# Kernel optimization log

Hardware: AMD Instinct MI355X
Metric: run time of the kernel (lower is better)

The kernel has to match this reference:

```python
import jax, jax.numpy as jnp
import numpy as np

NUM_HEADS = 16
HEAD_SIZE = 64
N_EMBD = 1024


def setup_inputs() -> dict:
    key = jax.random.key(0)
    ks = jax.random.split(key, 6)
    B, T, C = 2, 2048, N_EMBD
    scale = 0.02
    return {
        "x": jax.random.normal(ks[0], (B, T, C), dtype=jnp.float32),
        "Wq": jax.random.normal(ks[1], (C, NUM_HEADS * HEAD_SIZE), dtype=jnp.float32) * scale,
        "Wk": jax.random.normal(ks[2], (C, NUM_HEADS * HEAD_SIZE), dtype=jnp.float32) * scale,
        "Wv": jax.random.normal(ks[3], (C, NUM_HEADS * HEAD_SIZE), dtype=jnp.float32) * scale,
        "Wo": jax.random.normal(ks[4], (NUM_HEADS * HEAD_SIZE, C), dtype=jnp.float32) * scale,
        "bo": jnp.zeros((C,), dtype=jnp.float32),
    }


def reference(x, Wq, Wk, Wv, Wo, bo):
    B, T, C = x.shape
    H, D = NUM_HEADS, HEAD_SIZE
    # QKV projections (no bias), reshape to [B, H, T, D]
    q = (x @ Wq).reshape(B, T, H, D).transpose(0, 2, 1, 3)
    k = (x @ Wk).reshape(B, T, H, D).transpose(0, 2, 1, 3)
    v = (x @ Wv).reshape(B, T, H, D).transpose(0, 2, 1, 3)
    # scaled dot-product scores [B, H, T, T]
    scores = jnp.einsum("bhqd,bhkd->bhqk", q, k) / jnp.sqrt(jnp.float32(D))
    causal = jnp.tril(jnp.ones((T, T), dtype=bool))
    scores = jnp.where(causal, scores, -jnp.inf)
    weights = jax.nn.softmax(scores, axis=-1)  # dropout = identity (eval)
    out = jnp.einsum("bhqk,bhkd->bhqd", weights, v)
    out = out.transpose(0, 2, 1, 3).reshape(B, T, H * D)
    return out @ Wo + bo
```

## Files before the change

kernel.cpp:

```cpp
#include <hip/hip_runtime.h>

typedef __attribute__((ext_vector_type(8))) _Float16 f16x8;
typedef __attribute__((ext_vector_type(4))) _Float16 f16x4;
typedef __attribute__((ext_vector_type(2))) _Float16 f16x2;
typedef __attribute__((ext_vector_type(2))) __fp16   fp16x2_raw;
typedef __attribute__((ext_vector_type(4))) float    f32x4;

#define NUM_HEADS 16
#define HEAD_D 64
#define EMB 1024
#define SEQ 2048
#define BATCH 2
#define MTOT (BATCH * SEQ)

#define QALPHA 0.18033688011112042f

__device__ __forceinline__ f16x2 cvt_pk_f16(float lo, float hi)
{
    fp16x2_raw r = __builtin_amdgcn_cvt_pkrtz(lo, hi);
    return __builtin_bit_cast(f16x2, r);
}

#if defined(__has_builtin)
#if __has_builtin(__builtin_amdgcn_exp2f)
#define HAVE_EXP2 1
#endif
#endif
__device__ __forceinline__ float fast_exp2(float x)
{
#ifdef HAVE_EXP2
    return __builtin_amdgcn_exp2f(x);
#else
    return __expf(x * 0.6931471805599453f);
#endif
}

#if defined(__has_builtin)
#if __has_builtin(__builtin_amdgcn_global_load_lds)
#define HAVE_GLOAD_LDS 1
#endif
#endif

__device__ __forceinline__ void stage16(const void* g, void* ldsWaveBase, int lane)
{
#ifdef HAVE_GLOAD_LDS
    __builtin_amdgcn_global_load_lds(
        (const __attribute__((address_space(1))) void*)g,
        (__attribute__((address_space(3))) void*)ldsWaveBase, 16, 0, 0);
    (void)lane;
#else
    *(f16x8*)((char*)ldsWaveBase + lane * 16) = *(const f16x8*)g;
#endif
}

__global__ __launch_bounds__(256) void prep_all(
    const float* __restrict__ x,
    const float* __restrict__ Wq, const float* __restrict__ Wk,
    const float* __restrict__ Wv, const float* __restrict__ Wo,
    _Float16* __restrict__ xh, _Float16* __restrict__ Wt,
    _Float16* __restrict__ Wto)
{
    const int z = blockIdx.z;
    if (z == 4) {
        int base = ((blockIdx.y * 32 + blockIdx.x) * 256 + threadIdx.x) * 2;
        #pragma unroll
        for (int t = 0; t < 2; ++t) {
            int i = base + t;
            float4 a = ((const float4*)x)[i * 2];
            float4 b = ((const float4*)x)[i * 2 + 1];
            f16x8 o;
            o[0] = (_Float16)a.x; o[1] = (_Float16)a.y;
            o[2] = (_Float16)a.z; o[3] = (_Float16)a.w;
            o[4] = (_Float16)b.x; o[5] = (_Float16)b.y;
            o[6] = (_Float16)b.z; o[7] = (_Float16)b.w;
            ((f16x8*)xh)[i] = o;
        }
        return;
    }
    const float* W = z == 0 ? Wq : (z == 1 ? Wk : (z == 2 ? Wv : Wo));
    _Float16* D = (z == 3) ? Wto : (Wt + (size_t)z * EMB * EMB);
    __shared__ float tile[32][33];
    const int tx = threadIdx.x & 31, ty = threadIdx.x >> 5;
    const int n0 = blockIdx.x * 32, k0 = blockIdx.y * 32;
    #pragma unroll
    for (int j = 0; j < 4; ++j)
        tile[ty + j * 8][tx] = W[(size_t)(k0 + ty + j * 8) * EMB + n0 + tx];
    __syncthreads();
    #pragma unroll
    for (int j = 0; j < 4; ++j)
        D[(size_t)(n0 + ty + j * 8) * EMB + k0 + tx] =
            (_Float16)tile[tx][ty + j * 8];
}

__global__ __launch_bounds__(256) void gemm_qkv(
    const _Float16* __restrict__ A, const _Float16* __restrict__ Bt,
    _Float16* __restrict__ Qh, _Float16* __restrict__ Kh,
    _Float16* __restrict__ VhT)
{
    __shared__ __align__(16) _Float16 As[128 * 32];
    __shared__ __align__(16) _Float16 Bs[128 * 32];

    const int tid = threadIdx.x;
    const int w = tid >> 6, lane = tid & 63;
    const int l15 = lane & 15, g4 = lane >> 4;
    const int wm = w >> 1, wn = w & 1;

    const int wg = blockIdx.y * gridDim.x + blockIdx.x;
    const int t  = (wg & 7) * 96 + (wg >> 3);
    const int bx = t >> 5, by = t & 31;
    const int row0 = by * 128, col0 = bx * 128;

    f32x4 acc[4][4];
    #pragma unroll
    for (int mt = 0; mt < 4; ++mt)
        #pragma unroll
        for (int nt = 0; nt < 4; ++nt)
            acc[mt][nt] = (f32x4){0.f, 0.f, 0.f, 0.f};

    for (int k0 = 0; k0 < EMB; k0 += 32) {
        __syncthreads();
        #pragma unroll
        for (int i = 0; i < 2; ++i) {
            int c = (i << 8) + tid;
            int row = c >> 2, u = c & 3;
            stage16(&A[(size_t)(row0 + row) * EMB + k0 + (u << 3)],
                    (char*)As + (i << 12) + (w << 10), lane);
            stage16(&Bt[(size_t)(col0 + row) * EMB + k0 + (u << 3)],
                    (char*)Bs + (i << 12) + (w << 10), lane);
        }
        __syncthreads();

        f16x8 af[4], bf[4];
        #pragma unroll
        for (int mt = 0; mt < 4; ++mt)
            af[mt] = *(const f16x8*)((const char*)As +
                     ((wm << 6) + (mt << 4) + l15) * 64 + (g4 << 4));
        #pragma unroll
        for (int nt = 0; nt < 4; ++nt)
            bf[nt] = *(const f16x8*)((const char*)Bs +
                     ((wn << 6) + (nt << 4) + l15) * 64 + (g4 << 4));
        #pragma unroll
        for (int mt = 0; mt < 4; ++mt)
            #pragma unroll
            for (int nt = 0; nt < 4; ++nt)
                acc[mt][nt] = __builtin_amdgcn_mfma_f32_16x16x32_f16(
                    af[mt], bf[nt], acc[mt][nt], 0, 0, 0);
    }

    #pragma unroll
    for (int mt = 0; mt < 4; ++mt) {
        int m = row0 + (wm << 6) + (mt << 4) + (g4 << 2);
        #pragma unroll
        for (int nt = 0; nt < 4; ++nt) {
            int gcol = col0 + (wn << 6) + (nt << 4) + l15;
            int proj = gcol >> 10, pc = gcol & 1023;
            int h = pc >> 6, d = pc & 63;
            int b = m >> 11, tt = m & 2047;
            int bh = b * NUM_HEADS + h;
            if (proj == 2) {
                f16x4 v4;
                v4[0] = (_Float16)acc[mt][nt][0];
                v4[1] = (_Float16)acc[mt][nt][1];
                v4[2] = (_Float16)acc[mt][nt][2];
                v4[3] = (_Float16)acc[mt][nt][3];
                *(f16x4*)&VhT[((size_t)bh * HEAD_D + d) * SEQ + tt] = v4;
            } else {
                _Float16* dst = proj == 0 ? Qh : Kh;
                float alpha = proj == 0 ? QALPHA : 1.0f;
                #pragma unroll
                for (int r = 0; r < 4; ++r)
                    dst[((size_t)bh * SEQ + tt + r) * HEAD_D + d] =
                        (_Float16)(acc[mt][nt][r] * alpha);
            }
        }
    }
}

__global__ __launch_bounds__(256) void gemm_out(
    const _Float16* __restrict__ A, const _Float16* __restrict__ Bt,
    float* __restrict__ outf, const float* __restrict__ bias)
{
    __shared__ __align__(16) _Float16 As[128 * 32];
    __shared__ __align__(16) _Float16 Bs[64 * 32];

    const int tid = threadIdx.x;
    const int w = tid >> 6, lane = tid & 63;
    const int l15 = lane & 15, g4 = lane >> 4;
    const int wm = w >> 1, wn = w & 1;

    const int wg = blockIdx.y * gridDim.x + blockIdx.x;
    const int t  = (wg & 7) * 64 + (wg >> 3);
    const int bx = t >> 5, by = t & 31;
    const int row0 = by * 128, col0 = bx * 64;

    f32x4 acc[4][2];
    #pragma unroll
    for (int mt = 0; mt < 4; ++mt)
        #pragma unroll
        for (int nt = 0; nt < 2; ++nt)
            acc[mt][nt] = (f32x4){0.f, 0.f, 0.f, 0.f};

    for (int k0 = 0; k0 < EMB; k0 += 32) {
        __syncthreads();
        #pragma unroll
        for (int i = 0; i < 2; ++i) {
            int c = (i << 8) + tid;
            int row = c >> 2, u = c & 3;
            stage16(&A[(size_t)(row0 + row) * EMB + k0 + (u << 3)],
                    (char*)As + (i << 12) + (w << 10), lane);
        }
        {
            int row = tid >> 2, u = tid & 3;
            stage16(&Bt[(size_t)(col0 + row) * EMB + k0 + (u << 3)],
                    (char*)Bs + (w << 10), lane);
        }
        __syncthreads();

        f16x8 af[4], bf[2];
        #pragma unroll
        for (int mt = 0; mt < 4; ++mt)
            af[mt] = *(const f16x8*)((const char*)As +
                     ((wm << 6) + (mt << 4) + l15) * 64 + (g4 << 4));
        #pragma unroll
        for (int nt = 0; nt < 2; ++nt)
            bf[nt] = *(const f16x8*)((const char*)Bs +
                     ((wn << 5) + (nt << 4) + l15) * 64 + (g4 << 4));
        #pragma unroll
        for (int mt = 0; mt < 4; ++mt)
            #pragma unroll
            for (int nt = 0; nt < 2; ++nt)
                acc[mt][nt] = __builtin_amdgcn_mfma_f32_16x16x32_f16(
                    af[mt], bf[nt], acc[mt][nt], 0, 0, 0);
    }

    #pragma unroll
    for (int mt = 0; mt < 4; ++mt) {
        int m = row0 + (wm << 6) + (mt << 4) + (g4 << 2);
        #pragma unroll
        for (int nt = 0; nt < 2; ++nt) {
            int gcol = col0 + (wn << 5) + (nt << 4) + l15;
            float bz = bias[gcol];
            #pragma unroll
            for (int r = 0; r < 4; ++r)
                outf[(size_t)(m + r) * EMB + gcol] = acc[mt][nt][r] + bz;
        }
    }
}

__device__ __forceinline__ void stage_kv_tile(
    const _Float16* __restrict__ KhB, const _Float16* __restrict__ VtB,
    int kv0, char* __restrict__ KsBuf, char* __restrict__ VtBuf,
    int w, int lane)
{
    #pragma unroll
    for (int i = 0; i < 2; ++i) {
        int c = (i << 8) + (w << 6) + lane;
        int row = c >> 3, u = c & 7;
        int us = u ^ (row & 7);
        stage16(&KhB[(size_t)(kv0 + row) * HEAD_D + (us << 3)],
                KsBuf + (i << 12) + (w << 10), lane);
        stage16(&VtB[(size_t)row * SEQ + kv0 + (us << 3)],
                VtBuf + (i << 12) + (w << 10), lane);
    }
}

__device__ __forceinline__ void attn_tile(
    const char* __restrict__ KsC, const char* __restrict__ VtC,
    char* __restrict__ pwv,
    f16x8 qf0, f16x8 qf1, f32x4 (&acc)[4], float& m, float& l,
    bool diag, int qrel, int l15, int g)
{
    f32x4 st[4];
    #pragma unroll
    for (int nt = 0; nt < 4; ++nt) {
        int kvl = (nt << 4) + l15;
        f16x8 kf0 = *(const f16x8*)&KsC[kvl * 128 + (((g << 4)) ^ ((kvl & 7) << 4))];
        f16x8 kf1 = *(const f16x8*)&KsC[kvl * 128 + ((64 + (g << 4)) ^ ((kvl & 7) << 4))];
        f32x4 z = (f32x4){0.f, 0.f, 0.f, 0.f};
        z = __builtin_amdgcn_mfma_f32_16x16x32_f16(kf0, qf0, z, 0, 0, 0);
        z = __builtin_amdgcn_mfma_f32_16x16x32_f16(kf1, qf1, z, 0, 0, 0);
        st[nt] = z;
    }
    if (diag) {
        #pragma unroll
        for (int nt = 0; nt < 4; ++nt)
            #pragma unroll
            for (int r = 0; r < 4; ++r)
                if ((nt << 4) + (g << 2) + r > qrel) st[nt][r] = -1e30f;
    }

    float mx;
    {
        float a0 = fmaxf(fmaxf(st[0][0], st[0][1]), fmaxf(st[0][2], st[0][3]));
        float a1 = fmaxf(fmaxf(st[1][0], st[1][1]), fmaxf(st[1][2], st[1][3]));
        float a2 = fmaxf(fmaxf(st[2][0], st[2][1]), fmaxf(st[2][2], st[2][3]));
        float a3 = fmaxf(fmaxf(st[3][0], st[3][1]), fmaxf(st[3][2], st[3][3]));
        mx = fmaxf(fmaxf(a0, a1), fmaxf(a2, a3));
    }

    if (!__all(mx - m <= 8.0f)) {
        float mxr = fmaxf(mx, __shfl_xor(mx, 16));
        mxr = fmaxf(mxr, __shfl_xor(mxr, 32));
        float nm = fmaxf(m, mxr);
        float sc = fast_exp2(m - nm);
        m = nm;
        l *= sc;
        #pragma unroll
        for (int r = 0; r < 4; ++r) {
            float scr = __shfl(sc, (g << 2) + r);
            acc[0][r] *= scr; acc[1][r] *= scr;
            acc[2][r] *= scr; acc[3][r] *= scr;
        }
    }

    float ps = 0.f;
    #pragma unroll
    for (int nt = 0; nt < 4; ++nt)
        #pragma unroll
        for (int r = 0; r < 4; ++r) {
            float p = fast_exp2(st[nt][r] - m);
            st[nt][r] = p;
            ps += p;
        }
    l += ps;

    #pragma unroll
    for (int nt = 0; nt < 4; ++nt)
        #pragma unroll
        for (int rr = 0; rr < 2; ++rr) {
            int kvb = (nt << 4) + (g << 2) + (rr << 1);
            f16x2 pv = cvt_pk_f16(st[nt][rr * 2], st[nt][rr * 2 + 1]);
            *(f16x2*)&pwv[l15 * 128 + ((kvb << 1) ^ ((l15 & 7) << 4))] = pv;
        }
    f16x8 pa0 = *(const f16x8*)&pwv[l15 * 128 + (((g << 4)) ^ ((l15 & 7) << 4))];
    f16x8 pa1 = *(const f16x8*)&pwv[l15 * 128 + ((64 + (g << 4)) ^ ((l15 & 7) << 4))];

    #pragma unroll
    for (int dn = 0; dn < 4; ++dn) {
        int d = (dn << 4) + l15;
        f16x8 vf0 = *(const f16x8*)&VtC[d * 128 + (((g << 4)) ^ ((d & 7) << 4))];
        f16x8 vf1 = *(const f16x8*)&VtC[d * 128 + ((64 + (g << 4)) ^ ((d & 7) << 4))];
        acc[dn] = __builtin_amdgcn_mfma_f32_16x16x32_f16(pa0, vf0, acc[dn], 0, 0, 0);
        acc[dn] = __builtin_amdgcn_mfma_f32_16x16x32_f16(pa1, vf1, acc[dn], 0, 0, 0);
    }
}

__device__ __forceinline__ void attn_tile2(
    const char* __restrict__ Ks0, const char* __restrict__ Vt0,
    const char* __restrict__ Ks1, const char* __restrict__ Vt1,
    char* __restrict__ pwv0, char* __restrict__ pwv1,
    f16x8 qf0, f16x8 qf1, f32x4 (&acc)[4], float& m, float& l,
    bool diag1, int qrel, int l15, int g)
{
    f32x4 st[8];
    #pragma unroll
    for (int nt = 0; nt < 4; ++nt) {
        int kvl = (nt << 4) + l15;
        int off0 = kvl * 128 + (((g << 4)) ^ ((kvl & 7) << 4));
        int off1 = kvl * 128 + ((64 + (g << 4)) ^ ((kvl & 7) << 4));
        f16x8 ka0 = *(const f16x8*)&Ks0[off0];
        f16x8 ka1 = *(const f16x8*)&Ks0[off1];
        f32x4 z = (f32x4){0.f, 0.f, 0.f, 0.f};
        z = __builtin_amdgcn_mfma_f32_16x16x32_f16(ka0, qf0, z, 0, 0, 0);
        z = __builtin_amdgcn_mfma_f32_16x16x32_f16(ka1, qf1, z, 0, 0, 0);
        st[nt] = z;
        f16x8 kb0 = *(const f16x8*)&Ks1[off0];
        f16x8 kb1 = *(const f16x8*)&Ks1[off1];
        f32x4 z2 = (f32x4){0.f, 0.f, 0.f, 0.f};
        z2 = __builtin_amdgcn_mfma_f32_16x16x32_f16(kb0, qf0, z2, 0, 0, 0);
        z2 = __builtin_amdgcn_mfma_f32_16x16x32_f16(kb1, qf1, z2, 0, 0, 0);
        st[4 + nt] = z2;
    }
    if (diag1) {
        #pragma unroll
        for (int nt = 0; nt < 4; ++nt)
            #pragma unroll
            for (int r = 0; r < 4; ++r)
                if ((nt << 4) + (g << 2) + r > qrel) st[4 + nt][r] = -1e30f;
    }

    float mx;
    {
        float a = -1e30f;
        #pragma unroll
        for (int i = 0; i < 8; ++i)
            a = fmaxf(a, fmaxf(fmaxf(st[i][0], st[i][1]),
                               fmaxf(st[i][2], st[i][3])));
        mx = a;
    }

    if (!__all(mx - m <= 8.0f)) {
        float mxr = fmaxf(mx, __shfl_xor(mx, 16));
        mxr = fmaxf(mxr, __shfl_xor(mxr, 32));
        float nm = fmaxf(m, mxr);
        float sc = fast_exp2(m - nm);
        m = nm;
        l *= sc;
        #pragma unroll
        for (int r = 0; r < 4; ++r) {
            float scr = __shfl(sc, (g << 2) + r);
            acc[0][r] *= scr; acc[1][r] *= scr;
            acc[2][r] *= scr; acc[3][r] *= scr;
        }
    }

    float ps = 0.f;
    #pragma unroll
    for (int i = 0; i < 8; ++i)
        #pragma unroll
        for (int r = 0; r < 4; ++r) {
            float p = fast_exp2(st[i][r] - m);
            st[i][r] = p;
            ps += p;
        }
    l += ps;

    #pragma unroll
    for (int tile = 0; tile < 2; ++tile) {
        const f32x4* s4 = &st[tile << 2];
        const char* Vt = tile ? Vt1 : Vt0;
        char* pwv = tile ? pwv1 : pwv0;
        #pragma unroll
        for (int nt = 0; nt < 4; ++nt)
            #pragma unroll
            for (int rr = 0; rr < 2; ++rr) {
                int kvb = (nt << 4) + (g << 2) + (rr << 1);
                f16x2 pv = cvt_pk_f16(s4[nt][rr * 2], s4[nt][rr * 2 + 1]);
                *(f16x2*)&pwv[l15 * 128 + ((kvb << 1) ^ ((l15 & 7) << 4))] = pv;
            }
        f16x8 pa0 = *(const f16x8*)&pwv[l15 * 128 + (((g << 4)) ^ ((l15 & 7) << 4))];
        f16x8 pa1 = *(const f16x8*)&pwv[l15 * 128 + ((64 + (g << 4)) ^ ((l15 & 7) << 4))];
        #pragma unroll
        for (int dn = 0; dn < 4; ++dn) {
            int d = (dn << 4) + l15;
            f16x8 vf0 = *(const f16x8*)&Vt[d * 128 + (((g << 4)) ^ ((d & 7) << 4))];
            f16x8 vf1 = *(const f16x8*)&Vt[d * 128 + ((64 + (g << 4)) ^ ((d & 7) << 4))];
            acc[dn] = __builtin_amdgcn_mfma_f32_16x16x32_f16(pa0, vf0, acc[dn], 0, 0, 0);
            acc[dn] = __builtin_amdgcn_mfma_f32_16x16x32_f16(pa1, vf1, acc[dn], 0, 0, 0);
        }
    }
}

__global__ __launch_bounds__(256, 4) void attn_mfma(
    const _Float16* __restrict__ Qh, const _Float16* __restrict__ Kh,
    const _Float16* __restrict__ VhT, _Float16* __restrict__ O)
{
    __shared__ char lds[80 * 1024];
#define KSLOT(s) (lds + ((s) << 13))
#define VSLOT(s) (lds + 32768 + ((s) << 13))

    const int qtA = blockIdx.x;
    const int qtB = (SEQ / 64 - 1) - qtA;
    const int bh = blockIdx.y;
    const int q0A = qtA << 6, q0B = qtB << 6;
    const int tid = threadIdx.x;
    const int w = tid >> 6, lane = tid & 63;
    const int l15 = lane & 15, g = lane >> 4;

    const _Float16* KhB = Kh  + (size_t)bh * SEQ * HEAD_D;
    const _Float16* VtB = VhT + (size_t)bh * HEAD_D * SEQ;
    const size_t headbase = (size_t)bh * SEQ * HEAD_D;

    const int qrowA = q0A + (w << 4) + l15;
    const int qrowB = q0B + (w << 4) + l15;
    f16x8 qfA0 = *(const f16x8*)&Qh[headbase + (size_t)qrowA * HEAD_D + (g << 3)];
    f16x8 qfA1 = *(const f16x8*)&Qh[headbase + (size_t)qrowA * HEAD_D + 32 + (g << 3)];
    f16x8 qfB0 = *(const f16x8*)&Qh[headbase + (size_t)qrowB * HEAD_D + (g << 3)];
    f16x8 qfB1 = *(const f16x8*)&Qh[headbase + (size_t)qrowB * HEAD_D + 32 + (g << 3)];

    f32x4 accA[4], accB[4];
    #pragma unroll
    for (int dn = 0; dn < 4; ++dn) {
        accA[dn] = (f32x4){0.f, 0.f, 0.f, 0.f};
        accB[dn] = (f32x4){0.f, 0.f, 0.f, 0.f};
    }
    float mA = -1e30f, lA = 0.f, mB = -1e30f, lB = 0.f;

    stage_kv_tile(KhB, VtB, 0,  KSLOT(0), VSLOT(0), w, lane);
    stage_kv_tile(KhB, VtB, 64, KSLOT(1), VSLOT(1), w, lane);
    __syncthreads();

    char* pwvA = lds + 65536 + (w << 11);
    char* pwvB = lds + 73728 + (w << 11);
    const int qrel = (w << 4) + l15;

    for (int kt = 0; kt <= qtA; ++kt) {
        int pf = kt + 2;
        if (pf <= qtB)
            stage_kv_tile(KhB, VtB, pf << 6, KSLOT(pf & 3), VSLOT(pf & 3), w, lane);
        attn_tile(KSLOT(kt & 3), VSLOT(kt & 3), pwvA, qfA0, qfA1, accA, mA, lA,
                  kt == qtA, qrel, l15, g);
        attn_tile(KSLOT(kt & 3), VSLOT(kt & 3), pwvB, qfB0, qfB1, accB, mB, lB,
                  false, qrel, l15, g);
        __syncthreads();
    }

    {
        int kt = qtA + 1;
        int pf = kt + 2;
        if (pf <= qtB)
            stage_kv_tile(KhB, VtB, pf << 6, KSLOT(pf & 3), VSLOT(pf & 3), w, lane);
        attn_tile(KSLOT(kt & 3), VSLOT(kt & 3), pwvB, qfB0, qfB1, accB, mB, lB,
                  kt == qtB, qrel, l15, g);
        __syncthreads();
    }

    for (int kt = qtA + 2; kt < qtB; kt += 2) {
        int pf0 = kt + 2, pf1 = kt + 3;
        if (pf0 <= qtB)
            stage_kv_tile(KhB, VtB, pf0 << 6, KSLOT(pf0 & 3), VSLOT(pf0 & 3), w, lane);
        if (pf1 <= qtB)
            stage_kv_tile(KhB, VtB, pf1 << 6, KSLOT(pf1 & 3), VSLOT(pf1 & 3), w, lane);
        attn_tile2(KSLOT(kt & 3), VSLOT(kt & 3),
                   KSLOT((kt + 1) & 3), VSLOT((kt + 1) & 3),
                   pwvB, pwvA, qfB0, qfB1, accB, mB, lB,
                   (kt + 1) == qtB, qrel, l15, g);
        __syncthreads();
    }

    lA += __shfl_xor(lA, 16); lA += __shfl_xor(lA, 32);
    lB += __shfl_xor(lB, 16); lB += __shfl_xor(lB, 32);
    const int b = bh >> 4, h = bh & 15;
    const float rlA = 1.f / lA, rlB = 1.f / lB;
    #pragma unroll
    for (int r = 0; r < 4; ++r) {
        float invA = __shfl(rlA, (g << 2) + r);
        float invB = __shfl(rlB, (g << 2) + r);
        int tokA = (b << 11) + q0A + (w << 4) + (g << 2) + r;
        int tokB = (b << 11) + q0B + (w << 4) + (g << 2) + r;
        #pragma unroll
        for (int dn = 0; dn < 4; ++dn) {
            O[(size_t)tokA * EMB + (h << 6) + (dn << 4) + l15] =
                (_Float16)(accA[dn][r] * invA);
            O[(size_t)tokB * EMB + (h << 6) + (dn << 4) + l15] =
                (_Float16)(accB[dn][r] * invB);
        }
    }
#undef KSLOT
#undef VSLOT
}

extern "C" void kernel_launch(void* const* d_in, const int* in_sizes, int n_in,
                              void* d_out, int out_size, void* d_ws, size_t ws_size,
                              hipStream_t stream)
{
    const float* x  = (const float*)d_in[0];
    const float* Wq = (const float*)d_in[1];
    const float* Wk = (const float*)d_in[2];
    const float* Wv = (const float*)d_in[3];
    const float* Wo = (const float*)d_in[4];
    const float* bo = (const float*)d_in[5];
    float* out = (float*)d_out;

    const size_t ME = (size_t)MTOT * EMB;
    const size_t WE = (size_t)EMB * EMB;
    const size_t need = (5 * ME + 4 * WE) * sizeof(_Float16);
    if (ws_size < need) return;

    _Float16* xh  = (_Float16*)d_ws;
    _Float16* Wt  = xh + ME;
    _Float16* Wto = Wt + 3 * WE;
    _Float16* Qh  = Wto + WE;
    _Float16* Kh  = Qh + ME;
    _Float16* VhT = Kh + ME;
    _Float16* Ow  = VhT + ME;

    prep_all<<<dim3(EMB / 32, EMB / 32, 5), 256, 0, stream>>>(
        x, Wq, Wk, Wv, Wo, xh, Wt, Wto);

    gemm_qkv<<<dim3(3 * EMB / 128, MTOT / 128), 256, 0, stream>>>(
        xh, Wt, Qh, Kh, VhT);

    attn_mfma<<<dim3(SEQ / 128, BATCH * NUM_HEADS), 256, 0, stream>>>(Qh, Kh, VhT, Ow);

    gemm_out<<<dim3(EMB / 64, MTOT / 128), 256, 0, stream>>>(
        Ow, Wto, out, bo);
}
```

Measured before the change: 111.9 us.

## Double-buffer LDS tiles in QKV and output projection GEMMs

Both projection GEMMs now keep two LDS buffers per operand and issue the global-to-LDS copy of the next K-slice before running the MFMAs on the current one. This cuts the loop to a single barrier per iteration and is meant to overlap global load latency with matrix math. The cost is twice the shared memory per block, which could lower occupancy. Correctness depends on stage16 completing before the barrier; if it is an asynchronous LDS load, the wait semantics matter.

Result: slower. 119.1 us (+6.4%).

```diff
diff --git a/kernel.cpp b/kernel.cpp
--- a/kernel.cpp
+++ b/kernel.cpp
@@ -97,8 +97,8 @@
     _Float16* __restrict__ Qh, _Float16* __restrict__ Kh,
     _Float16* __restrict__ VhT)
 {
-    __shared__ __align__(16) _Float16 As[128 * 32];
-    __shared__ __align__(16) _Float16 Bs[128 * 32];
+    __shared__ __align__(16) _Float16 As[2][128 * 32];
+    __shared__ __align__(16) _Float16 Bs[2][128 * 32];
 
     const int tid = threadIdx.x;
     const int w = tid >> 6, lane = tid & 63;
@@ -117,27 +117,41 @@
         for (int nt = 0; nt < 4; ++nt)
             acc[mt][nt] = (f32x4){0.f, 0.f, 0.f, 0.f};
 
+    const int c0row = tid >> 2, c0u = tid & 3;
+    const int c1row = (256 + tid) >> 2, c1u = tid & 3;
+
+    stage16(&A[(size_t)(row0 + c0row) * EMB + (c0u << 3)],
+            (char*)As[0] + (w << 10), lane);
+    stage16(&Bt[(size_t)(col0 + c0row) * EMB + (c0u << 3)],
+            (char*)Bs[0] + (w << 10), lane);
+    stage16(&A[(size_t)(row0 + c1row) * EMB + (c1u << 3)],
+            (char*)As[0] + 4096 + (w << 10), lane);
+    stage16(&Bt[(size_t)(col0 + c1row) * EMB + (c1u << 3)],
+            (char*)Bs[0] + 4096 + (w << 10), lane);
+    __syncthreads();
+
+    int cur = 0;
     for (int k0 = 0; k0 < EMB; k0 += 32) {
-        __syncthreads();
-        #pragma unroll
-        for (int i = 0; i < 2; ++i) {
-            int c = (i << 8) + tid;
-            int row = c >> 2, u = c & 3;
-            stage16(&A[(size_t)(row0 + row) * EMB + k0 + (u << 3)],
-                    (char*)As + (i << 12) + (w << 10), lane);
-            stage16(&Bt[(size_t)(col0 + row) * EMB + k0 + (u << 3)],
-                    (char*)Bs + (i << 12) + (w << 10), lane);
-        }
-        __syncthreads();
+        if (k0 + 32 < EMB) {
+            int kn = k0 + 32;
+            stage16(&A[(size_t)(row0 + c0row) * EMB + kn + (c0u << 3)],
+                    (char*)As[cur ^ 1] + (w << 10), lane);
+            stage16(&Bt[(size_t)(col0 + c0row) * EMB + kn + (c0u << 3)],
+                    (char*)Bs[cur ^ 1] + (w << 10), lane);
+            stage16(&A[(size_t)(row0 + c1row) * EMB + kn + (c1u << 3)],
+                    (char*)As[cur ^ 1] + 4096 + (w << 10), lane);
+            stage16(&Bt[(size_t)(col0 + c1row) * EMB + kn + (c1u << 3)],
+                    (char*)Bs[cur ^ 1] + 4096 + (w << 10), lane);
+        }
 
         f16x8 af[4], bf[4];
         #pragma unroll
         for (int mt = 0; mt < 4; ++mt)
-            af[mt] = *(const f16x8*)((const char*)As +
+            af[mt] = *(const f16x8*)((const char*)As[cur] +
                      ((wm << 6) + (mt << 4) + l15) * 64 + (g4 << 4));
         #pragma unroll
         for (int nt = 0; nt < 4; ++nt)
-            bf[nt] = *(const f16x8*)((const char*)Bs +
+            bf[nt] = *(const f16x8*)((const char*)Bs[cur] +
                      ((wn << 6) + (nt << 4) + l15) * 64 + (g4 << 4));
         #pragma unroll
         for (int mt = 0; mt < 4; ++mt)
@@ -145,6 +159,9 @@
             for (int nt = 0; nt < 4; ++nt)
                 acc[mt][nt] = __builtin_amdgcn_mfma_f32_16x16x32_f16(
                     af[mt], bf[nt], acc[mt][nt], 0, 0, 0);
+
+        __syncthreads();
+        cur ^= 1;
     }
 
     #pragma unroll
@@ -180,8 +197,8 @@
     const _Float16* __restrict__ A, const _Float16* __restrict__ Bt,
     float* __restrict__ outf, const float* __restrict__ bias)
 {
-    __shared__ __align__(16) _Float16 As[128 * 32];
-    __shared__ __align__(16) _Float16 Bs[64 * 32];
+    __shared__ __align__(16) _Float16 As[2][128 * 32];
+    __shared__ __align__(16) _Float16 Bs[2][64 * 32];
 
     const int tid = threadIdx.x;
     const int w = tid >> 6, lane = tid & 63;
@@ -200,30 +217,37 @@
         for (int nt = 0; nt < 2; ++nt)
             acc[mt][nt] = (f32x4){0.f, 0.f, 0.f, 0.f};
 
+    const int c0row = tid >> 2, cu = tid & 3;
+    const int c1row = (256 + tid) >> 2;
+
+    stage16(&A[(size_t)(row0 + c0row) * EMB + (cu << 3)],
+            (char*)As[0] + (w << 10), lane);
+    stage16(&A[(size_t)(row0 + c1row) * EMB + (cu << 3)],
+            (char*)As[0] + 4096 + (w << 10), lane);
+    stage16(&Bt[(size_t)(col0 + c0row) * EMB + (cu << 3)],
+            (char*)Bs[0] + (w << 10), lane);
+    __syncthreads();
+
+    int cur = 0;
     for (int k0 = 0; k0 < EMB; k0 += 32) {
-        __syncthreads();
-        #pragma unroll
-        for (int i = 0; i < 2; ++i) {
-            int c = (i << 8) + tid;
-            int row = c >> 2, u = c & 3;
-            stage16(&A[(size_t)(row0 + row) * EMB + k0 + (u << 3)],
-                    (char*)As + (i << 12) + (w << 10), lane);
-        }
-        {
-            int row = tid >> 2, u = tid & 3;
-            stage16(&Bt[(size_t)(col0 + row) * EMB + k0 + (u << 3)],
-                    (char*)Bs + (w << 10), lane);
-        }
-        __syncthreads();
+        if (k0 + 32 < EMB) {
+            int kn = k0 + 32;
+            stage16(&A[(size_t)(row0 + c0row) * EMB + kn + (cu << 3)],
+                    (char*)As[cur ^ 1] + (w << 10), lane);
+            stage16(&A[(size_t)(row0 + c1row) * EMB + kn + (cu << 3)],
+                    (char*)As[cur ^ 1] + 4096 + (w << 10), lane);
+            stage16(&Bt[(size_t)(col0 + c0row) * EMB + kn + (cu << 3)],
+                    (char*)Bs[cur ^ 1] + (w << 10), lane);
+        }
 
         f16x8 af[4], bf[2];
         #pragma unroll
         for (int mt = 0; mt < 4; ++mt)
-            af[mt] = *(const f16x8*)((const char*)As +
+            af[mt] = *(const f16x8*)((const char*)As[cur] +
                      ((wm << 6) + (mt << 4) + l15) * 64 + (g4 << 4));
         #pragma unroll
         for (int nt = 0; nt < 2; ++nt)
-            bf[nt] = *(const f16x8*)((const char*)Bs +
+            bf[nt] = *(const f16x8*)((const char*)Bs[cur] +
                      ((wn << 5) + (nt << 4) + l15) * 64 + (g4 << 4));
         #pragma unroll
         for (int mt = 0; mt < 4; ++mt)
@@ -231,6 +255,9 @@
             for (int nt = 0; nt < 2; ++nt)
                 acc[mt][nt] = __builtin_amdgcn_mfma_f32_16x16x32_f16(
                     af[mt], bf[nt], acc[mt][nt], 0, 0, 0);
+
+        __syncthreads();
+        cur ^= 1;
     }
 
     #pragma unroll
```
